# Performance work log

Hardware: AMD Instinct MI355X
Metric: run time of the kernel (lower is better)

## Reference

```python
import jax, jax.numpy as jnp
import numpy as np

N = 100000
E = 6400000
H = 64  # hidden_nf


def setup_inputs() -> dict:
    key = jax.random.key(0)
    ks = jax.random.split(key, 12)
    x = jax.random.normal(ks[0], (N, 3), dtype=jnp.float32)
    vel = jax.random.normal(ks[1], (N, 3), dtype=jnp.float32)
    vel_norm = jax.random.uniform(ks[2], (N, 1), dtype=jnp.float32)
    edge_index = jax.random.randint(ks[3], (2, E), 0, N, dtype=jnp.int32)
    # coord_mlp_vel: Linear(1,H) -> LeakyReLU(0.2) -> Linear(H,1)
    W1 = jax.random.normal(ks[4], (H, 1), dtype=jnp.float32) * (1.0 / np.sqrt(1))
    b1 = jnp.zeros((H,), dtype=jnp.float32)
    W2 = jax.random.normal(ks[5], (1, H), dtype=jnp.float32) * (1.0 / np.sqrt(H))
    b2 = jnp.zeros((1,), dtype=jnp.float32)
    # phi: Linear(1,H) -> LeakyReLU(0.2) -> Linear(H,1,bias=False, xavier gain=0.001) -> Tanh
    Wp1 = jax.random.normal(ks[6], (H, 1), dtype=jnp.float32) * (1.0 / np.sqrt(1))
    bp1 = jnp.zeros((H,), dtype=jnp.float32)
    Wp2 = jax.random.normal(ks[7], (1, H), dtype=jnp.float32) * 0.001
    return {"x": x, "vel_norm": vel_norm, "vel": vel, "edge_index": edge_index,
            "W1": W1, "b1": b1, "W2": W2, "b2": b2,
            "Wp1": Wp1, "bp1": bp1, "Wp2": Wp2}


def reference(x, vel_norm, vel, edge_index, W1, b1, W2, b2, Wp1, bp1, Wp2):
    row, col = edge_index[0], edge_index[1]
    # edge_model: gather endpoint positions, radial distance -> tiny MLP -> scaled diff
    x_diff = x[row] - x[col]                                   # [E, 3]
    radial = jnp.sqrt(jnp.sum(x_diff * x_diff, axis=1, keepdims=True))  # [E, 1]
    h = jax.nn.leaky_relu(radial @ Wp1.T + bp1, 0.2)           # [E, H]
    e_out = jnp.tanh(h @ Wp2.T)                                # [E, 1]
    m_ij = x_diff * e_out                                      # [E, 3]
    # node_model: unsorted_segment_mean over row
    agg_sum = jax.ops.segment_sum(m_ij, row, num_segments=x.shape[0])           # [N, 3]
    cnt = jax.ops.segment_sum(jnp.ones((m_ij.shape[0], 1), m_ij.dtype), row,
                              num_segments=x.shape[0])                           # [N, 1]
    x_out = x + agg_sum / jnp.maximum(cnt, 1.0)
    # velocity term: x + vel * coord_mlp_vel(vel_norm)
    hv = jax.nn.leaky_relu(vel_norm @ W1.T + b1, 0.2)          # [N, H]
    scale = hv @ W2.T + b2                                     # [N, 1]
    return x_out + vel * scale
```

## Files before the change

### kernel.cpp

```cpp
#include <hip/hip_runtime.h>
#include <hip/hip_fp16.h>
#include <math.h>

#define LEAKY 0.2f
#define HDIM 64
#define EPB 2048
#define TPB1 256
#define PERT (EPB / TPB1)
#define RANGE 1024
#define RSH 10
#define KMAX 128
#define NSLICE 12
#define FIXS 4194304.0f
#define INVFIXS (1.0f / 4194304.0f)


__device__ __forceinline__ float fast_tanh(float v) {
    float e = __builtin_amdgcn_exp2f(v * 2.88539008178f);
    return 1.0f - 2.0f * __builtin_amdgcn_rcpf(e + 1.0f);
}

__device__ __forceinline__ float edge_eo(float rad, float C, bool slow,
                                         const float* sW1, const float* sb1,
                                         const float* sW2) {
    if (!slow) return fast_tanh(C * rad);
    float a = 0.f;
    #pragma unroll
    for (int k = 0; k < HDIM; k++) {
        float h = fmaf(rad, sW1[k], sb1[k]);
        h = (h > 0.f) ? h : LEAKY * h;
        a = fmaf(sW2[k], h, a);
    }
    return fast_tanh(a);
}

__global__ void repack_kernel(const float* __restrict__ x, float4* __restrict__ x4, int N) {
    int i = blockIdx.x * blockDim.x + threadIdx.x;
    if (i < N) x4[i] = make_float4(x[3*i], x[3*i+1], x[3*i+2], 0.f);
}

__global__ void repack_h_kernel(const float* __restrict__ x, uint2* __restrict__ xh, int N,
                                const float* __restrict__ Wp1, const float* __restrict__ bp1,
                                const float* __restrict__ Wp2, float* __restrict__ consts) {
    int i = blockIdx.x * blockDim.x + threadIdx.x;
    if (i < N) {
        unsigned hx = __half_as_ushort(__float2half(x[3*i]));
        unsigned hy = __half_as_ushort(__float2half(x[3*i+1]));
        unsigned hz = __half_as_ushort(__float2half(x[3*i+2]));
        xh[i] = make_uint2((hy << 16) | hx, hz);
    }
    if (blockIdx.x == 0 && threadIdx.x < 64) {
        int k = threadIdx.x;
        float w1 = Wp1[k];
        float slope = (w1 >= 0.f) ? 1.f : LEAKY;
        float c = Wp2[k] * w1 * slope;
        float bnz = (bp1[k] != 0.f) ? 1.f : 0.f;
        #pragma unroll
        for (int off = 32; off > 0; off >>= 1) {
            c += __shfl_down(c, off, 64);
            bnz += __shfl_down(bnz, off, 64);
        }
        if (k == 0) { consts[0] = c; consts[1] = bnz; }
    }
}

__device__ __forceinline__ unsigned long long pack_rec(float dx, float dy, float dz,
                                                       float eo, unsigned lid) {
    unsigned hx = __half_as_ushort(__float2half(dx * eo));
    unsigned hy = __half_as_ushort(__float2half(dy * eo));
    unsigned hz = __half_as_ushort(__float2half(dz * eo));
    return (unsigned long long)lid
         | ((unsigned long long)hx << 11)
         | ((unsigned long long)hy << 27)
         | ((unsigned long long)hz << 43);
}

__device__ __forceinline__ uint2 make_record(uint2 ga, uint2 gb, int r,
                                             float C, bool slow,
                                             const float* sW1, const float* sb1,
                                             const float* sW2) {
    float ax = __half2float(__ushort_as_half((unsigned short)(ga.x & 0xFFFF)));
    float ay = __half2float(__ushort_as_half((unsigned short)(ga.x >> 16)));
    float az = __half2float(__ushort_as_half((unsigned short)(ga.y & 0xFFFF)));
    float bx = __half2float(__ushort_as_half((unsigned short)(gb.x & 0xFFFF)));
    float by = __half2float(__ushort_as_half((unsigned short)(gb.x >> 16)));
    float bz = __half2float(__ushort_as_half((unsigned short)(gb.y & 0xFFFF)));
    float dx = ax - bx, dy = ay - by, dz = az - bz;
    float rad = sqrtf(dx*dx + dy*dy + dz*dz);
    float eo = edge_eo(rad, C, slow, sW1, sb1, sW2);
    unsigned long long u = pack_rec(dx, dy, dz, eo, (unsigned)r & (RANGE - 1));
    return make_uint2((unsigned)u, (unsigned)(u >> 32));
}

__global__ __launch_bounds__(TPB1) void count2_kernel(const int* __restrict__ ei,
                                                      unsigned* __restrict__ histG,
                                                      int E, int K) {
    __shared__ unsigned hist[4][KMAX];
    int w = threadIdx.x >> 6;
    for (int k = threadIdx.x; k < 4 * KMAX; k += TPB1) ((unsigned*)hist)[k] = 0;
    __syncthreads();
    const size_t base = (size_t)blockIdx.x * EPB;
    if (base + EPB <= (size_t)E) {
        const int4* p = (const int4*)(ei + base);
        #pragma unroll
        for (int i = 0; i < EPB / 4 / TPB1; i++) {
            int4 v = p[threadIdx.x + i * TPB1];
            atomicAdd(&hist[w][((unsigned)v.x) >> RSH], 1u);
            atomicAdd(&hist[w][((unsigned)v.y) >> RSH], 1u);
            atomicAdd(&hist[w][((unsigned)v.z) >> RSH], 1u);
            atomicAdd(&hist[w][((unsigned)v.w) >> RSH], 1u);
        }
    } else {
        for (size_t e = base + threadIdx.x; e < (size_t)E; e += TPB1)
            atomicAdd(&hist[w][((unsigned)ei[e]) >> RSH], 1u);
    }
    __syncthreads();
    for (int k = threadIdx.x; k < K; k += TPB1)
        histG[(size_t)blockIdx.x * K + k] = hist[0][k] + hist[1][k] + hist[2][k] + hist[3][k];
}

__global__ __launch_bounds__(256) void colscan_kernel(unsigned* __restrict__ histG,
                                                      unsigned* __restrict__ totals,
                                                      int nblk, int K) {
    __shared__ unsigned pa[256], pb[256];
    const int b = blockIdx.x;
    const int t = threadIdx.x;
    const int chunk = (nblk + 255) / 256;
    const int r0 = t * chunk;
    unsigned s = 0;
    for (int i = 0; i < chunk; i++) {
        int r = r0 + i;
        if (r < nblk) s += histG[(size_t)r * K + b];
    }
    pa[t] = s;
    __syncthreads();
    unsigned* src = pa; unsigned* dst = pb;
    for (int off = 1; off < 256; off <<= 1) {
        unsigned v = src[t];
        if (t >= off) v += src[t - off];
        dst[t] = v;
        __syncthreads();
        unsigned* tmp = src; src = dst; dst = tmp;
    }
    unsigned excl = (t > 0) ? src[t - 1] : 0u;
    if (t == 255) totals[b] = src[255];
    unsigned run = excl;
    for (int i = 0; i < chunk; i++) {
        int r = r0 + i;
        if (r < nblk) {
            size_t a = (size_t)r * K + b;
            unsigned v = histG[a];
            histG[a] = run;
            run += v;
        }
    }
}

__global__ __launch_bounds__(TPB1) void fused_kernel(
        const uint2* __restrict__ xh,
        const int* __restrict__ ei,
        const float* __restrict__ Wp1, const float* __restrict__ bp1,
        const float* __restrict__ Wp2, const float* __restrict__ consts,
        const unsigned* __restrict__ histG, const unsigned* __restrict__ totals,
        uint2* __restrict__ recs, int E, int K) {
    __shared__ uint2 stage[EPB];
    __shared__ unsigned char bucket_of[EPB];
    __shared__ unsigned hist[KMAX];
    __shared__ unsigned scanv[KMAX + 1];
    __shared__ unsigned gstart[KMAX];
    __shared__ unsigned sbase[KMAX + 1];
    __shared__ float sW1[HDIM], sb1[HDIM], sW2[HDIM];
    const float C = consts[0];
    const bool slow = (consts[1] != 0.f);
    if (slow) {
        for (int k = threadIdx.x; k < HDIM; k += TPB1) {
            sW1[k] = Wp1[k]; sb1[k] = bp1[k]; sW2[k] = Wp2[k];
        }
    }
    for (int k = threadIdx.x; k < K; k += TPB1) hist[k] = 0;
    if (threadIdx.x < (unsigned)K) sbase[threadIdx.x] = totals[threadIdx.x];
    __syncthreads();

    const size_t base = (size_t)blockIdx.x * EPB;
    const unsigned t = threadIdx.x;
    uint2 rc[PERT];
    unsigned bk[PERT];
    if (base + EPB <= (size_t)E && (E & 3) == 0) {
        const int4* pr = (const int4*)(ei + base);
        const int4* pc = (const int4*)(ei + (size_t)E + base);
        int4 rv0 = pr[t];
        int4 rv1 = pr[t + TPB1];
        int4 cv0 = pc[t];
        int4 cv1 = pc[t + TPB1];
        uint2 ga0 = xh[rv0.x], ga1 = xh[rv0.y], ga2 = xh[rv0.z], ga3 = xh[rv0.w];
        uint2 ga4 = xh[rv1.x], ga5 = xh[rv1.y], ga6 = xh[rv1.z], ga7 = xh[rv1.w];
        uint2 gb0 = xh[cv0.x], gb1 = xh[cv0.y], gb2 = xh[cv0.z], gb3 = xh[cv0.w];
        uint2 gb4 = xh[cv1.x], gb5 = xh[cv1.y], gb6 = xh[cv1.z], gb7 = xh[cv1.w];
        rc[0] = make_record(ga0, gb0, rv0.x, C, slow, sW1, sb1, sW2);
        rc[1] = make_record(ga1, gb1, rv0.y, C, slow, sW1, sb1, sW2);
        rc[2] = make_record(ga2, gb2, rv0.z, C, slow, sW1, sb1, sW2);
        rc[3] = make_record(ga3, gb3, rv0.w, C, slow, sW1, sb1, sW2);
        rc[4] = make_record(ga4, gb4, rv1.x, C, slow, sW1, sb1, sW2);
        rc[5] = make_record(ga5, gb5, rv1.y, C, slow, sW1, sb1, sW2);
        rc[6] = make_record(ga6, gb6, rv1.z, C, slow, sW1, sb1, sW2);
        rc[7] = make_record(ga7, gb7, rv1.w, C, slow, sW1, sb1, sW2);
        bk[0] = (unsigned)rv0.x >> RSH; bk[1] = (unsigned)rv0.y >> RSH;
        bk[2] = (unsigned)rv0.z >> RSH; bk[3] = (unsigned)rv0.w >> RSH;
        bk[4] = (unsigned)rv1.x >> RSH; bk[5] = (unsigned)rv1.y >> RSH;
        bk[6] = (unsigned)rv1.z >> RSH; bk[7] = (unsigned)rv1.w >> RSH;
        #pragma unroll
        for (int i = 0; i < PERT; i++) atomicAdd(&hist[bk[i]], 1u);
    } else {
        #pragma unroll
        for (int i = 0; i < PERT; i++) {
            size_t e = base + (size_t)i * TPB1 + t;
            bk[i] = 0xFFFFFFFFu;
            if (e < (size_t)E) {
                int r = ei[e];
                int c = ei[(size_t)E + e];
                uint2 ga = xh[r], gb = xh[c];
                rc[i] = make_record(ga, gb, r, C, slow, sW1, sb1, sW2);
                bk[i] = (unsigned)r >> RSH;
                atomicAdd(&hist[bk[i]], 1u);
            }
        }
    }
    __syncthreads();
    if (t == 0) {
        unsigned a = 0;
        for (int k = 0; k < K; k++) { scanv[k] = a; a += hist[k]; }
        scanv[K] = a;
    } else if (t == 64) {
        unsigned a = 0;
        for (int k = 0; k < K; k++) { unsigned v = sbase[k]; sbase[k] = a; a += v; }
        sbase[K] = a;
    }
    __syncthreads();
    if (t < (unsigned)K)
        gstart[t] = sbase[t] + histG[(size_t)blockIdx.x * K + t];
    for (int k = t; k < K; k += TPB1) hist[k] = scanv[k];
    __syncthreads();
    #pragma unroll
    for (int i = 0; i < PERT; i++) {
        if (bk[i] != 0xFFFFFFFFu) {
            unsigned slot = atomicAdd(&hist[bk[i]], 1u);
            stage[slot] = rc[i];
            bucket_of[slot] = (unsigned char)bk[i];
        }
    }
    __syncthreads();
    unsigned total = scanv[K];
    for (unsigned j = t; j < total; j += TPB1) {
        unsigned b_ = bucket_of[j];
        recs[(size_t)gstart[b_] + (j - scanv[b_])] = stage[j];
    }
}

__global__ __launch_bounds__(TPB1) void count_kernel(const int* __restrict__ ei,
                                                     unsigned* __restrict__ cnts,
                                                     int E, int K) {
    __shared__ unsigned hist[4][KMAX];
    int w = threadIdx.x >> 6;
    for (int k = threadIdx.x; k < 4 * KMAX; k += TPB1) ((unsigned*)hist)[k] = 0;
    __syncthreads();
    int base = blockIdx.x * EPB;
    #pragma unroll
    for (int i = 0; i < PERT; i++) {
        int e = base + i * TPB1 + threadIdx.x;
        if (e < E) atomicAdd(&hist[w][((unsigned)ei[e]) >> RSH], 1u);
    }
    __syncthreads();
    for (int k = threadIdx.x; k < K; k += TPB1) {
        unsigned t = hist[0][k] + hist[1][k] + hist[2][k] + hist[3][k];
        if (t) atomicAdd(&cnts[k], t);
    }
}

__global__ void scan_kernel(const unsigned* __restrict__ cnts,
                            unsigned* __restrict__ base,
                            unsigned* __restrict__ cursor, int K) {
    if (threadIdx.x == 0) {
        unsigned acc = 0;
        for (int k = 0; k < K; k++) { base[k] = acc; cursor[k] = acc; acc += cnts[k]; }
        base[K] = acc;
    }
}

__global__ void precompute_kernel(const float* __restrict__ Wp1,
                                  const float* __restrict__ bp1,
                                  const float* __restrict__ Wp2,
                                  float* __restrict__ consts) {
    int k = threadIdx.x;
    float w1 = Wp1[k];
    float slope = (w1 >= 0.f) ? 1.f : LEAKY;
    float c = Wp2[k] * w1 * slope;
    float bnz = (bp1[k] != 0.f) ? 1.f : 0.f;
    #pragma unroll
    for (int off = 32; off > 0; off >>= 1) {
        c += __shfl_down(c, off, 64);
        bnz += __shfl_down(bnz, off, 64);
    }
    if (k == 0) { consts[0] = c; consts[1] = bnz; }
}

__global__ __launch_bounds__(TPB1) void bin_kernel(
        const float* __restrict__ x, const float4* __restrict__ x4, int use4,
        const int* __restrict__ ei,
        const float* __restrict__ Wp1, const float* __restrict__ bp1,
        const float* __restrict__ Wp2, const float* __restrict__ consts,
        unsigned* __restrict__ cursor, uint2* __restrict__ recs, int E, int K) {
    __shared__ uint2 stage[EPB];
    __shared__ unsigned char bucket_of[EPB];
    __shared__ unsigned hist[KMAX];
    __shared__ unsigned scanv[KMAX + 1];
    __shared__ unsigned gstart[KMAX];
    __shared__ float sW1[HDIM], sb1[HDIM], sW2[HDIM];
    const float C = consts[0];
    const bool slow = (consts[1] != 0.f);
    if (slow) {
        for (int k = threadIdx.x; k < HDIM; k += TPB1) {
            sW1[k] = Wp1[k]; sb1[k] = bp1[k]; sW2[k] = Wp2[k];
        }
    }
    for (int k = threadIdx.x; k < K; k += TPB1) hist[k] = 0;
    __syncthreads();

    int base = blockIdx.x * EPB;
    uint2 rc[PERT];
    unsigned bk[PERT];
    #pragma unroll
    for (int i = 0; i < PERT; i++) {
        int e = base + i * TPB1 + threadIdx.x;
        bk[i] = 0xFFFFFFFFu;
        if (e < E) {
            int r = ei[e];
            int c = ei[(size_t)E + e];
            float dx, dy, dz;
            if (use4) {
                float4 a = x4[r], b = x4[c];
                dx = a.x - b.x; dy = a.y - b.y; dz = a.z - b.z;
            } else {
                dx = x[3*r]   - x[3*c];
                dy = x[3*r+1] - x[3*c+1];
                dz = x[3*r+2] - x[3*c+2];
            }
            float rad = sqrtf(dx*dx + dy*dy + dz*dz);
            float eo = edge_eo(rad, C, slow, sW1, sb1, sW2);
            unsigned long long u = pack_rec(dx, dy, dz, eo, (unsigned)r & (RANGE - 1));
            rc[i] = make_uint2((unsigned)u, (unsigned)(u >> 32));
            bk[i] = (unsigned)r >> RSH;
            atomicAdd(&hist[bk[i]], 1u);
        }
    }
    __syncthreads();
    if (threadIdx.x == 0) {
        unsigned a = 0;
        for (int k = 0; k < K; k++) { scanv[k] = a; a += hist[k]; }
        scanv[K] = a;
    }
    __syncthreads();
    if (threadIdx.x < (unsigned)K) {
        unsigned c_ = scanv[threadIdx.x + 1] - scanv[threadIdx.x];
        gstart[threadIdx.x] = c_ ? atomicAdd(&cursor[threadIdx.x], c_) : 0u;
    }
    for (int k = threadIdx.x; k < K; k += TPB1) hist[k] = scanv[k];
    __syncthreads();
    #pragma unroll
    for (int i = 0; i < PERT; i++) {
        if (bk[i] != 0xFFFFFFFFu) {
            unsigned slot = atomicAdd(&hist[bk[i]], 1u);
            stage[slot] = rc[i];
            bucket_of[slot] = (unsigned char)bk[i];
        }
    }
    __syncthreads();
    unsigned total = scanv[K];
    for (unsigned j = threadIdx.x; j < total; j += TPB1) {
        unsigned b_ = bucket_of[j];
        recs[(size_t)gstart[b_] + (j - scanv[b_])] = stage[j];
    }
}

__device__ __forceinline__ void proc_rec(uint2 r, unsigned (*acc)[RANGE]) {
    unsigned long long u = ((unsigned long long)r.y << 32) | r.x;
    unsigned lid = (unsigned)(u & (RANGE - 1));
    float mx = __half2float(__ushort_as_half((unsigned short)((u >> 11) & 0xFFFF)));
    float my = __half2float(__ushort_as_half((unsigned short)((u >> 27) & 0xFFFF)));
    float mz = __half2float(__ushort_as_half((unsigned short)((u >> 43) & 0xFFFF)));
    atomicAdd(&acc[0][lid], (unsigned)(int)__float2int_rn(mx * FIXS));
    atomicAdd(&acc[1][lid], (unsigned)(int)__float2int_rn(my * FIXS));
    atomicAdd(&acc[2][lid], (unsigned)(int)__float2int_rn(mz * FIXS));
    atomicAdd(&acc[3][lid], 1u);
}

__global__ __launch_bounds__(256) void reduce_kernel(
        const uint2* __restrict__ recs, const unsigned* __restrict__ totals,
        float4* __restrict__ slices, int N, int K) {
    __shared__ unsigned acc[4][RANGE];
    __shared__ unsigned sbase[KMAX + 1];
    int b = blockIdx.x / NSLICE;
    int s = blockIdx.x % NSLICE;
    if (threadIdx.x < (unsigned)K) sbase[threadIdx.x] = totals[threadIdx.x];
    for (int i = threadIdx.x; i < RANGE; i += 256) {
        acc[0][i] = 0u; acc[1][i] = 0u; acc[2][i] = 0u; acc[3][i] = 0u;
    }
    __syncthreads();
    if (threadIdx.x == 0) {
        unsigned a = 0;
        for (int k = 0; k < K; k++) { unsigned v = sbase[k]; sbase[k] = a; a += v; }
        sbase[K] = a;
    }
    __syncthreads();
    unsigned lo = sbase[b], hi = sbase[b + 1];
    unsigned cnt = hi - lo;
    unsigned per = (cnt + NSLICE - 1) / NSLICE;
    unsigned st = lo + (unsigned)s * per;
    unsigned en = st + per; if (en > hi) en = hi;
    unsigned j = st + threadIdx.x;
    if (st < hi) {
        while (j + 256 < en) {
            uint2 r0 = recs[j];
            uint2 r1 = recs[j + 256];
            proc_rec(r0, acc);
            proc_rec(r1, acc);
            j += 512;
        }
        while (j < en) { proc_rec(recs[j], acc); j += 256; }
    }
    __syncthreads();
    int nbase = b * RANGE;
    for (int i = threadIdx.x; i < RANGE; i += 256) {
        int node = nbase + i;
        if (node < N)
            slices[(size_t)s * N + node] =
                make_float4((float)(int)acc[0][i] * INVFIXS,
                            (float)(int)acc[1][i] * INVFIXS,
                            (float)(int)acc[2][i] * INVFIXS,
                            (float)acc[3][i]);
    }
}

__global__ void node_kernel(const float* __restrict__ x, const float* __restrict__ vel_norm,
                            const float* __restrict__ vel,
                            const float* __restrict__ W1, const float* __restrict__ b1,
                            const float* __restrict__ W2, const float* __restrict__ b2,
                            const float4* __restrict__ slices,
                            float* __restrict__ out, int N, int S) {
    __shared__ float sW1[HDIM], sb1[HDIM], sW2[HDIM];
    for (int k = threadIdx.x; k < HDIM; k += blockDim.x) {
        sW1[k] = W1[k]; sb1[k] = b1[k]; sW2[k] = W2[k];
    }
    __syncthreads();
    int i = blockIdx.x * blockDim.x + threadIdx.x;
    if (i >= N) return;
    float sx = 0.f, sy = 0.f, sz = 0.f, sc = 0.f;
    for (int s = 0; s < S; s++) {
        float4 v = slices[(size_t)s * N + i];
        sx += v.x; sy += v.y; sz += v.z; sc += v.w;
    }
    float vn = vel_norm[i];
    float a = b2[0];
    #pragma unroll
    for (int k = 0; k < HDIM; k++) {
        float h = fmaf(vn, sW1[k], sb1[k]);
        h = (h > 0.f) ? h : LEAKY * h;
        a = fmaf(sW2[k], h, a);
    }
    float inv = 1.0f / fmaxf(sc, 1.0f);
    out[3*i]     = x[3*i]     + sx * inv + vel[3*i]     * a;
    out[3*i + 1] = x[3*i + 1] + sy * inv + vel[3*i + 1] * a;
    out[3*i + 2] = x[3*i + 2] + sz * inv + vel[3*i + 2] * a;
}

__global__ __launch_bounds__(256) void reduce_basep_kernel(
        const uint2* __restrict__ recs, const unsigned* __restrict__ base,
        float4* __restrict__ slices, int N, int K) {
    __shared__ unsigned acc[4][RANGE];
    int b = blockIdx.x / NSLICE;
    int s = blockIdx.x % NSLICE;
    for (int i = threadIdx.x; i < RANGE; i += 256) {
        acc[0][i] = 0u; acc[1][i] = 0u; acc[2][i] = 0u; acc[3][i] = 0u;
    }
    __syncthreads();
    unsigned lo = base[b], hi = base[b + 1];
    unsigned cnt = hi - lo;
    unsigned per = (cnt + NSLICE - 1) / NSLICE;
    unsigned st = lo + (unsigned)s * per;
    unsigned en = st + per; if (en > hi) en = hi;
    unsigned j = st + threadIdx.x;
    if (st < hi) {
        while (j + 256 < en) {
            uint2 r0 = recs[j];
            uint2 r1 = recs[j + 256];
            proc_rec(r0, acc);
            proc_rec(r1, acc);
            j += 512;
        }
        while (j < en) { proc_rec(recs[j], acc); j += 256; }
    }
    __syncthreads();
    int nbase = b * RANGE;
    for (int i = threadIdx.x; i < RANGE; i += 256) {
        int node = nbase + i;
        if (node < N)
            slices[(size_t)s * N + node] =
                make_float4((float)(int)acc[0][i] * INVFIXS,
                            (float)(int)acc[1][i] * INVFIXS,
                            (float)(int)acc[2][i] * INVFIXS,
                            (float)acc[3][i]);
    }
}

__global__ void edge_atomic_kernel(const float* __restrict__ x, const int* __restrict__ ei,
                                   const float* __restrict__ Wp1, const float* __restrict__ bp1,
                                   const float* __restrict__ Wp2, const float* __restrict__ consts,
                                   float* __restrict__ acc, int E) {
    __shared__ float sW1[HDIM], sb1[HDIM], sW2[HDIM];
    const float C = consts[0];
    const bool slow = (consts[1] != 0.f);
    if (slow) {
        for (int k = threadIdx.x; k < HDIM; k += blockDim.x) {
            sW1[k] = Wp1[k]; sb1[k] = bp1[k]; sW2[k] = Wp2[k];
        }
        __syncthreads();
    }
    int e = blockIdx.x * blockDim.x + threadIdx.x;
    if (e >= E) return;
    int r = ei[e];
    int c = ei[E + e];
    float dx = x[3*r] - x[3*c];
    float dy = x[3*r+1] - x[3*c+1];
    float dz = x[3*r+2] - x[3*c+2];
    float rad = sqrtf(dx*dx + dy*dy + dz*dz);
    float eo = edge_eo(rad, C, slow, sW1, sb1, sW2);
    float* basep = acc + ((size_t)r << 2);
    atomicAdd(basep + 0, dx * eo);
    atomicAdd(basep + 1, dy * eo);
    atomicAdd(basep + 2, dz * eo);
    atomicAdd(basep + 3, 1.f);
}

extern "C" void kernel_launch(void* const* d_in, const int* in_sizes, int n_in,
                              void* d_out, int out_size, void* d_ws, size_t ws_size,
                              hipStream_t stream) {
    const float* x        = (const float*)d_in[0];
    const float* vel_norm = (const float*)d_in[1];
    const float* vel      = (const float*)d_in[2];
    const int*   ei       = (const int*)  d_in[3];
    const float* W1       = (const float*)d_in[4];
    const float* b1       = (const float*)d_in[5];
    const float* W2       = (const float*)d_in[6];
    const float* b2       = (const float*)d_in[7];
    const float* Wp1      = (const float*)d_in[8];
    const float* bp1      = (const float*)d_in[9];
    const float* Wp2      = (const float*)d_in[10];

    const int N = in_sizes[0] / 3;
    const int E = in_sizes[3] / 2;
    const int K = (N + RANGE - 1) / RANGE;
    const int nblk = (E + EPB - 1) / EPB;

    size_t rec_bytes   = (size_t)E * sizeof(uint2);
    size_t slice_bytes = (size_t)NSLICE * N * sizeof(float4);
    size_t x4_bytes    = (size_t)N * sizeof(float4);
    size_t histG_bytes = (size_t)nblk * K * sizeof(unsigned);

    size_t sp_slices = rec_bytes;
    size_t sp_xh     = sp_slices + slice_bytes;
    size_t sp_hist   = sp_xh + x4_bytes;
    size_t sp_tot    = sp_hist + histG_bytes;
    size_t sp_const  = (sp_tot + (size_t)(K + 1) * sizeof(unsigned) + 15) & ~(size_t)15;
    size_t need_split = sp_const + 32;

    size_t small_bytes = (size_t)(KMAX + (KMAX + 1) + KMAX) * sizeof(unsigned) + 32;
    size_t fu_recs  = slice_bytes;
    size_t fu_x4    = fu_recs + rec_bytes;
    size_t fu_small = fu_x4 + x4_bytes;
    size_t need_fused = fu_small + small_bytes;

    if (K <= KMAX && ws_size >= need_split) {
        uint2*    recs   = (uint2*)   d_ws;
        float4*   slices = (float4*)  ((char*)d_ws + sp_slices);
        uint2*    xh     = (uint2*)   ((char*)d_ws + sp_xh);
        unsigned* histG  = (unsigned*)((char*)d_ws + sp_hist);
        unsigned* totals = (unsigned*)((char*)d_ws + sp_tot);
        float*    consts = (float*)   ((char*)d_ws + sp_const);

        repack_h_kernel<<<(N + 255) / 256, 256, 0, stream>>>(x, xh, N, Wp1, bp1, Wp2, consts);
        count2_kernel<<<nblk, TPB1, 0, stream>>>(ei, histG, E, K);
        colscan_kernel<<<K, 256, 0, stream>>>(histG, totals, nblk, K);
        fused_kernel<<<nblk, TPB1, 0, stream>>>(xh, ei, Wp1, bp1, Wp2, consts,
                                                histG, totals, recs, E, K);
        reduce_kernel<<<K * NSLICE, 256, 0, stream>>>(recs, totals, slices, N, K);
        node_kernel<<<(N + 255) / 256, 256, 0, stream>>>(x, vel_norm, vel, W1, b1, W2, b2,
                                                         slices, (float*)d_out, N, NSLICE);
    } else if (K <= KMAX && ws_size >= need_fused) {
        float4*   slices = (float4*)  d_ws;
        uint2*    recs   = (uint2*)   ((char*)d_ws + fu_recs);
        float4*   x4     = (float4*)  ((char*)d_ws + fu_x4);
        unsigned* cnts   = (unsigned*)((char*)d_ws + fu_small);
        unsigned* basep  = cnts + KMAX;
        unsigned* cursor = basep + KMAX + 1;
        float*    consts = (float*)(cursor + KMAX);

        hipMemsetAsync(cnts, 0, small_bytes, stream);
        precompute_kernel<<<1, 64, 0, stream>>>(Wp1, bp1, Wp2, consts);
        repack_kernel<<<(N + 255) / 256, 256, 0, stream>>>(x, x4, N);
        count_kernel<<<nblk, TPB1, 0, stream>>>(ei, cnts, E, K);
        scan_kernel<<<1, 64, 0, stream>>>(cnts, basep, cursor, K);
        bin_kernel<<<nblk, TPB1, 0, stream>>>(x, x4, 1, ei, Wp1, bp1, Wp2, consts,
                                              cursor, recs, E, K);
        reduce_basep_kernel<<<K * NSLICE, 256, 0, stream>>>(recs, basep, slices, N, K);
        node_kernel<<<(N + 255) / 256, 256, 0, stream>>>(x, vel_norm, vel, W1, b1, W2, b2,
                                                         slices, (float*)d_out, N, NSLICE);
    } else {
        float* acc    = (float*)d_ws;
        float* consts = (float*)((char*)d_ws + (size_t)N * sizeof(float4));
        hipMemsetAsync(d_ws, 0, (size_t)N * sizeof(float4) + 32, stream);
        precompute_kernel<<<1, 64, 0, stream>>>(Wp1, bp1, Wp2, consts);
        edge_atomic_kernel<<<(E + 255) / 256, 256, 0, stream>>>(x, ei, Wp1, bp1, Wp2,
                                                                consts, acc, E);
        node_kernel<<<(N + 255) / 256, 256, 0, stream>>>(x, vel_norm, vel, W1, b1, W2, b2,
                                                         (const float4*)acc, (float*)d_out, N, 1);
    }
}
```

Measured before the change: 201.4 us.

## Replace count/scan passes with fixed-capacity buckets and atomic cursors

Removes the separate edge-count histogram kernel and the column scan. Each bucket now gets a fixed-capacity region, and every block claims its offset with a global atomic cursor. Edges that overflow a bucket are accumulated straight into a global fixed-point accumulator. The reduce kernel now atomically adds its per-bucket shared sums into a single N-sized integer accumulator instead of writing per-slice float4 arrays, so the node kernel reads one uint4 per node. This saves a full read of the edge index and two launches, at the cost of global atomics and a record order that depends on timing (integer sums stay deterministic).

```diff
diff --git a/kernel.cpp b/kernel.cpp
--- a/kernel.cpp
+++ b/kernel.cpp
@@ -34,33 +34,33 @@
     return fast_tanh(a);
 }
 
-__global__ void repack_kernel(const float* __restrict__ x, float4* __restrict__ x4, int N) {
-    int i = blockIdx.x * blockDim.x + threadIdx.x;
-    if (i < N) x4[i] = make_float4(x[3*i], x[3*i+1], x[3*i+2], 0.f);
-}
-
 __global__ void repack_h_kernel(const float* __restrict__ x, uint2* __restrict__ xh, int N,
                                 const float* __restrict__ Wp1, const float* __restrict__ bp1,
-                                const float* __restrict__ Wp2, float* __restrict__ consts) {
+                                const float* __restrict__ Wp2, float* __restrict__ consts,
+                                uint4* __restrict__ acc4, unsigned* __restrict__ cursor, int K) {
     int i = blockIdx.x * blockDim.x + threadIdx.x;
     if (i < N) {
         unsigned hx = __half_as_ushort(__float2half(x[3*i]));
         unsigned hy = __half_as_ushort(__float2half(x[3*i+1]));
         unsigned hz = __half_as_ushort(__float2half(x[3*i+2]));
         xh[i] = make_uint2((hy << 16) | hx, hz);
-    }
-    if (blockIdx.x == 0 && threadIdx.x < 64) {
-        int k = threadIdx.x;
-        float w1 = Wp1[k];
-        float slope = (w1 >= 0.f) ? 1.f : LEAKY;
-        float c = Wp2[k] * w1 * slope;
-        float bnz = (bp1[k] != 0.f) ? 1.f : 0.f;
-        #pragma unroll
-        for (int off = 32; off > 0; off >>= 1) {
-            c += __shfl_down(c, off, 64);
-            bnz += __shfl_down(bnz, off, 64);
-        }
-        if (k == 0) { consts[0] = c; consts[1] = bnz; }
+        acc4[i] = make_uint4(0u, 0u, 0u, 0u);
+    }
+    if (blockIdx.x == 0) {
+        if (threadIdx.x < 64) {
+            int k = threadIdx.x;
+            float w1 = Wp1[k];
+            float slope = (w1 >= 0.f) ? 1.f : LEAKY;
+            float c = Wp2[k] * w1 * slope;
+            float bnz = (bp1[k] != 0.f) ? 1.f : 0.f;
+            #pragma unroll
+            for (int off = 32; off > 0; off >>= 1) {
+                c += __shfl_down(c, off, 64);
+                bnz += __shfl_down(bnz, off, 64);
+            }
+            if (k == 0) { consts[0] = c; consts[1] = bnz; }
+        }
+        if ((int)threadIdx.x < K) cursor[threadIdx.x] = 0u;
     }
 }
 
@@ -92,83 +92,31 @@
     return make_uint2((unsigned)u, (unsigned)(u >> 32));
 }
 
-__global__ __launch_bounds__(TPB1) void count2_kernel(const int* __restrict__ ei,
-                                                      unsigned* __restrict__ histG,
-                                                      int E, int K) {
-    __shared__ unsigned hist[4][KMAX];
-    int w = threadIdx.x >> 6;
-    for (int k = threadIdx.x; k < 4 * KMAX; k += TPB1) ((unsigned*)hist)[k] = 0;
-    __syncthreads();
-    const size_t base = (size_t)blockIdx.x * EPB;
-    if (base + EPB <= (size_t)E) {
-        const int4* p = (const int4*)(ei + base);
-        #pragma unroll
-        for (int i = 0; i < EPB / 4 / TPB1; i++) {
-            int4 v = p[threadIdx.x + i * TPB1];
-            atomicAdd(&hist[w][((unsigned)v.x) >> RSH], 1u);
-            atomicAdd(&hist[w][((unsigned)v.y) >> RSH], 1u);
-            atomicAdd(&hist[w][((unsigned)v.z) >> RSH], 1u);
-            atomicAdd(&hist[w][((unsigned)v.w) >> RSH], 1u);
-        }
-    } else {
-        for (size_t e = base + threadIdx.x; e < (size_t)E; e += TPB1)
-            atomicAdd(&hist[w][((unsigned)ei[e]) >> RSH], 1u);
-    }
-    __syncthreads();
-    for (int k = threadIdx.x; k < K; k += TPB1)
-        histG[(size_t)blockIdx.x * K + k] = hist[0][k] + hist[1][k] + hist[2][k] + hist[3][k];
-}
-
-__global__ __launch_bounds__(256) void colscan_kernel(unsigned* __restrict__ histG,
-                                                      unsigned* __restrict__ totals,
-                                                      int nblk, int K) {
-    __shared__ unsigned pa[256], pb[256];
-    const int b = blockIdx.x;
-    const int t = threadIdx.x;
-    const int chunk = (nblk + 255) / 256;
-    const int r0 = t * chunk;
-    unsigned s = 0;
-    for (int i = 0; i < chunk; i++) {
-        int r = r0 + i;
-        if (r < nblk) s += histG[(size_t)r * K + b];
-    }
-    pa[t] = s;
-    __syncthreads();
-    unsigned* src = pa; unsigned* dst = pb;
-    for (int off = 1; off < 256; off <<= 1) {
-        unsigned v = src[t];
-        if (t >= off) v += src[t - off];
-        dst[t] = v;
-        __syncthreads();
-        unsigned* tmp = src; src = dst; dst = tmp;
-    }
-    unsigned excl = (t > 0) ? src[t - 1] : 0u;
-    if (t == 255) totals[b] = src[255];
-    unsigned run = excl;
-    for (int i = 0; i < chunk; i++) {
-        int r = r0 + i;
-        if (r < nblk) {
-            size_t a = (size_t)r * K + b;
-            unsigned v = histG[a];
-            histG[a] = run;
-            run += v;
-        }
-    }
-}
-
-__global__ __launch_bounds__(TPB1) void fused_kernel(
+__device__ __forceinline__ void rec_to_acc4(uint2 r, unsigned b_, unsigned* acc4) {
+    unsigned long long u = ((unsigned long long)r.y << 32) | r.x;
+    unsigned lid = (unsigned)(u & (RANGE - 1));
+    unsigned node = b_ * RANGE + lid;
+    float mx = __half2float(__ushort_as_half((unsigned short)((u >> 11) & 0xFFFF)));
+    float my = __half2float(__ushort_as_half((unsigned short)((u >> 27) & 0xFFFF)));
+    float mz = __half2float(__ushort_as_half((unsigned short)((u >> 43) & 0xFFFF)));
+    atomicAdd(&acc4[4*node + 0], (unsigned)(int)__float2int_rn(mx * FIXS));
+    atomicAdd(&acc4[4*node + 1], (unsigned)(int)__float2int_rn(my * FIXS));
+    atomicAdd(&acc4[4*node + 2], (unsigned)(int)__float2int_rn(mz * FIXS));
+    atomicAdd(&acc4[4*node + 3], 1u);
+}
+
+__global__ __launch_bounds__(TPB1) void fused3_kernel(
         const uint2* __restrict__ xh,
         const int* __restrict__ ei,
         const float* __restrict__ Wp1, const float* __restrict__ bp1,
         const float* __restrict__ Wp2, const float* __restrict__ consts,
-        const unsigned* __restrict__ histG, const unsigned* __restrict__ totals,
-        uint2* __restrict__ recs, int E, int K) {
+        unsigned* __restrict__ cursor, unsigned* __restrict__ acc4,
+        uint2* __restrict__ recs, int E, int K, unsigned cap) {
     __shared__ uint2 stage[EPB];
     __shared__ unsigned char bucket_of[EPB];
     __shared__ unsigned hist[KMAX];
     __shared__ unsigned scanv[KMAX + 1];
     __shared__ unsigned gstart[KMAX];
-    __shared__ unsigned sbase[KMAX + 1];
     __shared__ float sW1[HDIM], sb1[HDIM], sW2[HDIM];
     const float C = consts[0];
     const bool slow = (consts[1] != 0.f);
@@ -178,7 +126,6 @@
         }
     }
     for (int k = threadIdx.x; k < K; k += TPB1) hist[k] = 0;
-    if (threadIdx.x < (unsigned)K) sbase[threadIdx.x] = totals[threadIdx.x];
     __syncthreads();
 
     const size_t base = (size_t)blockIdx.x * EPB;
@@ -230,14 +177,12 @@
         unsigned a = 0;
         for (int k = 0; k < K; k++) { scanv[k] = a; a += hist[k]; }
         scanv[K] = a;
-    } else if (t == 64) {
-        unsigned a = 0;
-        for (int k = 0; k < K; k++) { unsigned v = sbase[k]; sbase[k] = a; a += v; }
-        sbase[K] = a;
-    }
-    __syncthreads();
-    if (t < (unsigned)K)
-        gstart[t] = sbase[t] + histG[(size_t)blockIdx.x * K + t];
+    }
+    __syncthreads();
+    if (t < (unsigned)K) {
+        unsigned c_ = scanv[t + 1] - scanv[t];
+        gstart[t] = c_ ? atomicAdd(&cursor[t], c_) : 0u;
+    }
     for (int k = t; k < K; k += TPB1) hist[k] = scanv[k];
     __syncthreads();
     #pragma unroll
@@ -252,38 +197,95 @@
     unsigned total = scanv[K];
     for (unsigned j = t; j < total; j += TPB1) {
         unsigned b_ = bucket_of[j];
-        recs[(size_t)gstart[b_] + (j - scanv[b_])] = stage[j];
-    }
-}
-
-__global__ __launch_bounds__(TPB1) void count_kernel(const int* __restrict__ ei,
-                                                     unsigned* __restrict__ cnts,
-                                                     int E, int K) {
-    __shared__ unsigned hist[4][KMAX];
-    int w = threadIdx.x >> 6;
-    for (int k = threadIdx.x; k < 4 * KMAX; k += TPB1) ((unsigned*)hist)[k] = 0;
-    __syncthreads();
-    int base = blockIdx.x * EPB;
+        unsigned off = gstart[b_] + (j - scanv[b_]);
+        if (off < cap) recs[(size_t)b_ * cap + off] = stage[j];
+        else           rec_to_acc4(stage[j], b_, acc4);
+    }
+}
+
+__device__ __forceinline__ void proc_rec(uint2 r, unsigned (*acc)[RANGE]) {
+    unsigned long long u = ((unsigned long long)r.y << 32) | r.x;
+    unsigned lid = (unsigned)(u & (RANGE - 1));
+    float mx = __half2float(__ushort_as_half((unsigned short)((u >> 11) & 0xFFFF)));
+    float my = __half2float(__ushort_as_half((unsigned short)((u >> 27) & 0xFFFF)));
+    float mz = __half2float(__ushort_as_half((unsigned short)((u >> 43) & 0xFFFF)));
+    atomicAdd(&acc[0][lid], (unsigned)(int)__float2int_rn(mx * FIXS));
+    atomicAdd(&acc[1][lid], (unsigned)(int)__float2int_rn(my * FIXS));
+    atomicAdd(&acc[2][lid], (unsigned)(int)__float2int_rn(mz * FIXS));
+    atomicAdd(&acc[3][lid], 1u);
+}
+
+__global__ __launch_bounds__(256) void reduce3_kernel(
+        const uint2* __restrict__ recs, const unsigned* __restrict__ cursor,
+        unsigned* __restrict__ acc4, int N, int K, unsigned cap) {
+    __shared__ unsigned acc[4][RANGE];
+    int b = blockIdx.x / NSLICE;
+    int s = blockIdx.x % NSLICE;
+    for (int i = threadIdx.x; i < RANGE; i += 256) {
+        acc[0][i] = 0u; acc[1][i] = 0u; acc[2][i] = 0u; acc[3][i] = 0u;
+    }
+    __syncthreads();
+    unsigned cnt = cursor[b];
+    if (cnt > cap) cnt = cap;
+    unsigned per = (cnt + NSLICE - 1) / NSLICE;
+    unsigned st = (unsigned)s * per;
+    unsigned en = st + per; if (en > cnt) en = cnt;
+    const uint2* rb = recs + (size_t)b * cap;
+    unsigned j = st + threadIdx.x;
+    if (st < cnt) {
+        while (j + 256 < en) {
+            uint2 r0 = rb[j];
+            uint2 r1 = rb[j + 256];
+            proc_rec(r0, acc);
+            proc_rec(r1, acc);
+            j += 512;
+        }
+        while (j < en) { proc_rec(rb[j], acc); j += 256; }
+    }
+    __syncthreads();
+    int nbase = b * RANGE;
+    for (int i = threadIdx.x; i < RANGE; i += 256) {
+        int node = nbase + i;
+        if (node < N && acc[3][i] != 0u) {
+            atomicAdd(&acc4[4*node + 0], acc[0][i]);
+            atomicAdd(&acc4[4*node + 1], acc[1][i]);
+            atomicAdd(&acc4[4*node + 2], acc[2][i]);
+            atomicAdd(&acc4[4*node + 3], acc[3][i]);
+        }
+    }
+}
+
+__global__ void node_fixed_kernel(const float* __restrict__ x,
+                                  const float* __restrict__ vel_norm,
+                                  const float* __restrict__ vel,
+                                  const float* __restrict__ W1, const float* __restrict__ b1,
+                                  const float* __restrict__ W2, const float* __restrict__ b2,
+                                  const uint4* __restrict__ acc4,
+                                  float* __restrict__ out, int N) {
+    __shared__ float sW1[HDIM], sb1[HDIM], sW2[HDIM];
+    for (int k = threadIdx.x; k < HDIM; k += blockDim.x) {
+        sW1[k] = W1[k]; sb1[k] = b1[k]; sW2[k] = W2[k];
+    }
+    __syncthreads();
+    int i = blockIdx.x * blockDim.x + threadIdx.x;
+    if (i >= N) return;
+    uint4 a4 = acc4[i];
+    float sx = (float)(int)a4.x * INVFIXS;
+    float sy = (float)(int)a4.y * INVFIXS;
+    float sz = (float)(int)a4.z * INVFIXS;
+    float sc = (float)a4.w;
+    float vn = vel_norm[i];
+    float a = b2[0];
     #pragma unroll
-    for (int i = 0; i < PERT; i++) {
-        int e = base + i * TPB1 + threadIdx.x;
-        if (e < E) atomicAdd(&hist[w][((unsigned)ei[e]) >> RSH], 1u);
-    }
-    __syncthreads();
-    for (int k = threadIdx.x; k < K; k += TPB1) {
-        unsigned t = hist[0][k] + hist[1][k] + hist[2][k] + hist[3][k];
-        if (t) atomicAdd(&cnts[k], t);
-    }
-}
-
-__global__ void scan_kernel(const unsigned* __restrict__ cnts,
-                            unsigned* __restrict__ base,
-                            unsigned* __restrict__ cursor, int K) {
-    if (threadIdx.x == 0) {
-        unsigned acc = 0;
-        for (int k = 0; k < K; k++) { base[k] = acc; cursor[k] = acc; acc += cnts[k]; }
-        base[K] = acc;
-    }
+    for (int k = 0; k < HDIM; k++) {
+        float h = fmaf(vn, sW1[k], sb1[k]);
+        h = (h > 0.f) ? h : LEAKY * h;
+        a = fmaf(sW2[k], h, a);
+    }
+    float inv = 1.0f / fmaxf(sc, 1.0f);
+    out[3*i]     = x[3*i]     + sx * inv + vel[3*i]     * a;
+    out[3*i + 1] = x[3*i + 1] + sy * inv + vel[3*i + 1] * a;
+    out[3*i + 2] = x[3*i + 2] + sz * inv + vel[3*i + 2] * a;
 }
 
 __global__ void precompute_kernel(const float* __restrict__ Wp1,
@@ -301,214 +303,6 @@
         bnz += __shfl_down(bnz, off, 64);
     }
     if (k == 0) { consts[0] = c; consts[1] = bnz; }
-}
-
-__global__ __launch_bounds__(TPB1) void bin_kernel(
-        const float* __restrict__ x, const float4* __restrict__ x4, int use4,
-        const int* __restrict__ ei,
-        const float* __restrict__ Wp1, const float* __restrict__ bp1,
-        const float* __restrict__ Wp2, const float* __restrict__ consts,
-        unsigned* __restrict__ cursor, uint2* __restrict__ recs, int E, int K) {
-    __shared__ uint2 stage[EPB];
-    __shared__ unsigned char bucket_of[EPB];
-    __shared__ unsigned hist[KMAX];
-    __shared__ unsigned scanv[KMAX + 1];
-    __shared__ unsigned gstart[KMAX];
-    __shared__ float sW1[HDIM], sb1[HDIM], sW2[HDIM];
-    const float C = consts[0];
-    const bool slow = (consts[1] != 0.f);
-    if (slow) {
-        for (int k = threadIdx.x; k < HDIM; k += TPB1) {
-            sW1[k] = Wp1[k]; sb1[k] = bp1[k]; sW2[k] = Wp2[k];
-        }
-    }
-    for (int k = threadIdx.x; k < K; k += TPB1) hist[k] = 0;
-    __syncthreads();
-
-    int base = blockIdx.x * EPB;
-    uint2 rc[PERT];
-    unsigned bk[PERT];
-    #pragma unroll
-    for (int i = 0; i < PERT; i++) {
-        int e = base + i * TPB1 + threadIdx.x;
-        bk[i] = 0xFFFFFFFFu;
-        if (e < E) {
-            int r = ei[e];
-            int c = ei[(size_t)E + e];
-            float dx, dy, dz;
-            if (use4) {
-                float4 a = x4[r], b = x4[c];
-                dx = a.x - b.x; dy = a.y - b.y; dz = a.z - b.z;
-            } else {
-                dx = x[3*r]   - x[3*c];
-                dy = x[3*r+1] - x[3*c+1];
-                dz = x[3*r+2] - x[3*c+2];
-            }
-            float rad = sqrtf(dx*dx + dy*dy + dz*dz);
-            float eo = edge_eo(rad, C, slow, sW1, sb1, sW2);
-            unsigned long long u = pack_rec(dx, dy, dz, eo, (unsigned)r & (RANGE - 1));
-            rc[i] = make_uint2((unsigned)u, (unsigned)(u >> 32));
-            bk[i] = (unsigned)r >> RSH;
-            atomicAdd(&hist[bk[i]], 1u);
-        }
-    }
-    __syncthreads();
-    if (threadIdx.x == 0) {
-        unsigned a = 0;
-        for (int k = 0; k < K; k++) { scanv[k] = a; a += hist[k]; }
-        scanv[K] = a;
-    }
-    __syncthreads();
-    if (threadIdx.x < (unsigned)K) {
-        unsigned c_ = scanv[threadIdx.x + 1] - scanv[threadIdx.x];
-        gstart[threadIdx.x] = c_ ? atomicAdd(&cursor[threadIdx.x], c_) : 0u;
-    }
-    for (int k = threadIdx.x; k < K; k += TPB1) hist[k] = scanv[k];
-    __syncthreads();
-    #pragma unroll
-    for (int i = 0; i < PERT; i++) {
-        if (bk[i] != 0xFFFFFFFFu) {
-            unsigned slot = atomicAdd(&hist[bk[i]], 1u);
-            stage[slot] = rc[i];
-            bucket_of[slot] = (unsigned char)bk[i];
-        }
-    }
-    __syncthreads();
-    unsigned total = scanv[K];
-    for (unsigned j = threadIdx.x; j < total; j += TPB1) {
-        unsigned b_ = bucket_of[j];
-        recs[(size_t)gstart[b_] + (j - scanv[b_])] = stage[j];
-    }
-}
-
-__device__ __forceinline__ void proc_rec(uint2 r, unsigned (*acc)[RANGE]) {
-    unsigned long long u = ((unsigned long long)r.y << 32) | r.x;
-    unsigned lid = (unsigned)(u & (RANGE - 1));
-    float mx = __half2float(__ushort_as_half((unsigned short)((u >> 11) & 0xFFFF)));
-    float my = __half2float(__ushort_as_half((unsigned short)((u >> 27) & 0xFFFF)));
-    float mz = __half2float(__ushort_as_half((unsigned short)((u >> 43) & 0xFFFF)));
-    atomicAdd(&acc[0][lid], (unsigned)(int)__float2int_rn(mx * FIXS));
-    atomicAdd(&acc[1][lid], (unsigned)(int)__float2int_rn(my * FIXS));
-    atomicAdd(&acc[2][lid], (unsigned)(int)__float2int_rn(mz * FIXS));
-    atomicAdd(&acc[3][lid], 1u);
-}
-
-__global__ __launch_bounds__(256) void reduce_kernel(
-        const uint2* __restrict__ recs, const unsigned* __restrict__ totals,
-        float4* __restrict__ slices, int N, int K) {
-    __shared__ unsigned acc[4][RANGE];
-    __shared__ unsigned sbase[KMAX + 1];
-    int b = blockIdx.x / NSLICE;
-    int s = blockIdx.x % NSLICE;
-    if (threadIdx.x < (unsigned)K) sbase[threadIdx.x] = totals[threadIdx.x];
-    for (int i = threadIdx.x; i < RANGE; i += 256) {
-        acc[0][i] = 0u; acc[1][i] = 0u; acc[2][i] = 0u; acc[3][i] = 0u;
-    }
-    __syncthreads();
-    if (threadIdx.x == 0) {
-        unsigned a = 0;
-        for (int k = 0; k < K; k++) { unsigned v = sbase[k]; sbase[k] = a; a += v; }
-        sbase[K] = a;
-    }
-    __syncthreads();
-    unsigned lo = sbase[b], hi = sbase[b + 1];
-    unsigned cnt = hi - lo;
-    unsigned per = (cnt + NSLICE - 1) / NSLICE;
-    unsigned st = lo + (unsigned)s * per;
-    unsigned en = st + per; if (en > hi) en = hi;
-    unsigned j = st + threadIdx.x;
-    if (st < hi) {
-        while (j + 256 < en) {
-            uint2 r0 = recs[j];
-            uint2 r1 = recs[j + 256];
-            proc_rec(r0, acc);
-            proc_rec(r1, acc);
-            j += 512;
-        }
-        while (j < en) { proc_rec(recs[j], acc); j += 256; }
-    }
-    __syncthreads();
-    int nbase = b * RANGE;
-    for (int i = threadIdx.x; i < RANGE; i += 256) {
-        int node = nbase + i;
-        if (node < N)
-            slices[(size_t)s * N + node] =
-                make_float4((float)(int)acc[0][i] * INVFIXS,
-                            (float)(int)acc[1][i] * INVFIXS,
-                            (float)(int)acc[2][i] * INVFIXS,
-                            (float)acc[3][i]);
-    }
-}
-
-__global__ void node_kernel(const float* __restrict__ x, const float* __restrict__ vel_norm,
-                            const float* __restrict__ vel,
-                            const float* __restrict__ W1, const float* __restrict__ b1,
-                            const float* __restrict__ W2, const float* __restrict__ b2,
-                            const float4* __restrict__ slices,
-                            float* __restrict__ out, int N, int S) {
-    __shared__ float sW1[HDIM], sb1[HDIM], sW2[HDIM];
-    for (int k = threadIdx.x; k < HDIM; k += blockDim.x) {
-        sW1[k] = W1[k]; sb1[k] = b1[k]; sW2[k] = W2[k];
-    }
-    __syncthreads();
-    int i = blockIdx.x * blockDim.x + threadIdx.x;
-    if (i >= N) return;
-    float sx = 0.f, sy = 0.f, sz = 0.f, sc = 0.f;
-    for (int s = 0; s < S; s++) {
-        float4 v = slices[(size_t)s * N + i];
-        sx += v.x; sy += v.y; sz += v.z; sc += v.w;
-    }
-    float vn = vel_norm[i];
-    float a = b2[0];
-    #pragma unroll
-    for (int k = 0; k < HDIM; k++) {
-        float h = fmaf(vn, sW1[k], sb1[k]);
-        h = (h > 0.f) ? h : LEAKY * h;
-        a = fmaf(sW2[k], h, a);
-    }
-    float inv = 1.0f / fmaxf(sc, 1.0f);
-    out[3*i]     = x[3*i]     + sx * inv + vel[3*i]     * a;
-    out[3*i + 1] = x[3*i + 1] + sy * inv + vel[3*i + 1] * a;
-    out[3*i + 2] = x[3*i + 2] + sz * inv + vel[3*i + 2] * a;
-}
-
-__global__ __launch_bounds__(256) void reduce_basep_kernel(
-        const uint2* __restrict__ recs, const unsigned* __restrict__ base,
-        float4* __restrict__ slices, int N, int K) {
-    __shared__ unsigned acc[4][RANGE];
-    int b = blockIdx.x / NSLICE;
-    int s = blockIdx.x % NSLICE;
-    for (int i = threadIdx.x; i < RANGE; i += 256) {
-        acc[0][i] = 0u; acc[1][i] = 0u; acc[2][i] = 0u; acc[3][i] = 0u;
-    }
-    __syncthreads();
-    unsigned lo = base[b], hi = base[b + 1];
-    unsigned cnt = hi - lo;
-    unsigned per = (cnt + NSLICE - 1) / NSLICE;
-    unsigned st = lo + (unsigned)s * per;
-    unsigned en = st + per; if (en > hi) en = hi;
-    unsigned j = st + threadIdx.x;
-    if (st < hi) {
-        while (j + 256 < en) {
-            uint2 r0 = recs[j];
-            uint2 r1 = recs[j + 256];
-            proc_rec(r0, acc);
-            proc_rec(r1, acc);
-            j += 512;
-        }
-        while (j < en) { proc_rec(recs[j], acc); j += 256; }
-    }
-    __syncthreads();
-    int nbase = b * RANGE;
-    for (int i = threadIdx.x; i < RANGE; i += 256) {
-        int node = nbase + i;
-        if (node < N)
-            slices[(size_t)s * N + node] =
-                make_float4((float)(int)acc[0][i] * INVFIXS,
-                            (float)(int)acc[1][i] * INVFIXS,
-                            (float)(int)acc[2][i] * INVFIXS,
-                            (float)acc[3][i]);
-    }
 }
 
 __global__ void edge_atomic_kernel(const float* __restrict__ x, const int* __restrict__ ei,
@@ -540,6 +334,38 @@
     atomicAdd(basep + 3, 1.f);
 }
 
+__global__ void node_kernel(const float* __restrict__ x, const float* __restrict__ vel_norm,
+                            const float* __restrict__ vel,
+                            const float* __restrict__ W1, const float* __restrict__ b1,
+                            const float* __restrict__ W2, const float* __restrict__ b2,
+                            const float4* __restrict__ slices,
+                            float* __restrict__ out, int N, int S) {
+    __shared__ float sW1[HDIM], sb1[HDIM], sW2[HDIM];
+    for (int k = threadIdx.x; k < HDIM; k += blockDim.x) {
+        sW1[k] = W1[k]; sb1[k] = b1[k]; sW2[k] = W2[k];
+    }
+    __syncthreads();
+    int i = blockIdx.x * blockDim.x + threadIdx.x;
+    if (i >= N) return;
+    float sx = 0.f, sy = 0.f, sz = 0.f, sc = 0.f;
+    for (int s = 0; s < S; s++) {
+        float4 v = slices[(size_t)s * N + i];
+        sx += v.x; sy += v.y; sz += v.z; sc += v.w;
+    }
+    float vn = vel_norm[i];
+    float a = b2[0];
+    #pragma unroll
+    for (int k = 0; k < HDIM; k++) {
+        float h = fmaf(vn, sW1[k], sb1[k]);
+        h = (h > 0.f) ? h : LEAKY * h;
+        a = fmaf(sW2[k], h, a);
+    }
+    float inv = 1.0f / fmaxf(sc, 1.0f);
+    out[3*i]     = x[3*i]     + sx * inv + vel[3*i]     * a;
+    out[3*i + 1] = x[3*i + 1] + sy * inv + vel[3*i + 1] * a;
+    out[3*i + 2] = x[3*i + 2] + sz * inv + vel[3*i + 2] * a;
+}
+
 extern "C" void kernel_launch(void* const* d_in, const int* in_sizes, int n_in,
                               void* d_out, int out_size, void* d_ws, size_t ws_size,
                               hipStream_t stream) {
@@ -560,59 +386,29 @@
     const int K = (N + RANGE - 1) / RANGE;
     const int nblk = (E + EPB - 1) / EPB;
 
-    size_t rec_bytes   = (size_t)E * sizeof(uint2);
-    size_t slice_bytes = (size_t)NSLICE * N * sizeof(float4);
-    size_t x4_bytes    = (size_t)N * sizeof(float4);
-    size_t histG_bytes = (size_t)nblk * K * sizeof(unsigned);
-
-    size_t sp_slices = rec_bytes;
-    size_t sp_xh     = sp_slices + slice_bytes;
-    size_t sp_hist   = sp_xh + x4_bytes;
-    size_t sp_tot    = sp_hist + histG_bytes;
-    size_t sp_const  = (sp_tot + (size_t)(K + 1) * sizeof(unsigned) + 15) & ~(size_t)15;
-    size_t need_split = sp_const + 32;
-
-    size_t small_bytes = (size_t)(KMAX + (KMAX + 1) + KMAX) * sizeof(unsigned) + 32;
-    size_t fu_recs  = slice_bytes;
-    size_t fu_x4    = fu_recs + rec_bytes;
-    size_t fu_small = fu_x4 + x4_bytes;
-    size_t need_fused = fu_small + small_bytes;
-
-    if (K <= KMAX && ws_size >= need_split) {
+    unsigned cap = (unsigned)((E + K - 1) / K) + 8192u;
+    cap = (cap + 63u) & ~63u;
+
+    size_t sp_xh    = (size_t)K * cap * sizeof(uint2);
+    size_t sp_acc   = (sp_xh + (size_t)N * sizeof(uint2) + 15) & ~(size_t)15;
+    size_t sp_cur   = sp_acc + (size_t)N * sizeof(uint4);
+    size_t sp_const = (sp_cur + (size_t)KMAX * sizeof(unsigned) + 15) & ~(size_t)15;
+    size_t need     = sp_const + 32;
+
+    if (K <= KMAX && ws_size >= need) {
         uint2*    recs   = (uint2*)   d_ws;
-        float4*   slices = (float4*)  ((char*)d_ws + sp_slices);
         uint2*    xh     = (uint2*)   ((char*)d_ws + sp_xh);
-        unsigned* histG  = (unsigned*)((char*)d_ws + sp_hist);
-        unsigned* totals = (unsigned*)((char*)d_ws + sp_tot);
+        unsigned* acc4   = (unsigned*)((char*)d_ws + sp_acc);
+        unsigned* cursor = (unsigned*)((char*)d_ws + sp_cur);
         float*    consts = (float*)   ((char*)d_ws + sp_const);
 
-        repack_h_kernel<<<(N + 255) / 256, 256, 0, stream>>>(x, xh, N, Wp1, bp1, Wp2, consts);
-        count2_kernel<<<nblk, TPB1, 0, stream>>>(ei, histG, E, K);
-        colscan_kernel<<<K, 256, 0, stream>>>(histG, totals, nblk, K);
-        fused_kernel<<<nblk, TPB1, 0, stream>>>(xh, ei, Wp1, bp1, Wp2, consts,
-                                                histG, totals, recs, E, K);
-        reduce_kernel<<<K * NSLICE, 256, 0, stream>>>(recs, totals, slices, N, K);
-        node_kernel<<<(N + 255) / 256, 256, 0, stream>>>(x, vel_norm, vel, W1, b1, W2, b2,
-                                                         slices, (float*)d_out, N, NSLICE);
-    } else if (K <= KMAX && ws_size >= need_fused) {
-        float4*   slices = (float4*)  d_ws;
-        uint2*    recs   = (uint2*)   ((char*)d_ws + fu_recs);
-        float4*   x4     = (float4*)  ((char*)d_ws + fu_x4);
-        unsigned* cnts   = (unsigned*)((char*)d_ws + fu_small);
-        unsigned* basep  = cnts + KMAX;
-        unsigned* cursor = basep + KMAX + 1;
-        float*    consts = (float*)(cursor + KMAX);
-
-        hipMemsetAsync(cnts, 0, small_bytes, stream);
-        precompute_kernel<<<1, 64, 0, stream>>>(Wp1, bp1, Wp2, consts);
-        repack_kernel<<<(N + 255) / 256, 256, 0, stream>>>(x, x4, N);
-        count_kernel<<<nblk, TPB1, 0, stream>>>(ei, cnts, E, K);
-        scan_kernel<<<1, 64, 0, stream>>>(cnts, basep, cursor, K);
-        bin_kernel<<<nblk, TPB1, 0, stream>>>(x, x4, 1, ei, Wp1, bp1, Wp2, consts,
-                                              cursor, recs, E, K);
-        reduce_basep_kernel<<<K * NSLICE, 256, 0, stream>>>(recs, basep, slices, N, K);
-        node_kernel<<<(N + 255) / 256, 256, 0, stream>>>(x, vel_norm, vel, W1, b1, W2, b2,
-                                                         slices, (float*)d_out, N, NSLICE);
+        repack_h_kernel<<<(N + 255) / 256, 256, 0, stream>>>(
+            x, xh, N, Wp1, bp1, Wp2, consts, (uint4*)acc4, cursor, K);
+        fused3_kernel<<<nblk, TPB1, 0, stream>>>(
+            xh, ei, Wp1, bp1, Wp2, consts, cursor, acc4, recs, E, K, cap);
+        reduce3_kernel<<<K * NSLICE, 256, 0, stream>>>(recs, cursor, acc4, N, K, cap);
+        node_fixed_kernel<<<(N + 255) / 256, 256, 0, stream>>>(
+            x, vel_norm, vel, W1, b1, W2, b2, (const uint4*)acc4, (float*)d_out, N);
     } else {
         float* acc    = (float*)d_ws;
         float* consts = (float*)((char*)d_ws + (size_t)N * sizeof(float4));
```

Result: slower. 237.1 us (+17.8%).
